# Performance work log

Hardware: AMD Instinct MI355X
Metric: run time of the kernel (lower is better)

## Reference

```python
import jax, jax.numpy as jnp
import numpy as np

SIGMA = 1e-4      # cone height (DistanceFieldPenetrationLoss sigma)
EPS = 1e-9
THRESH = 2000.0   # pen_loss[pen_loss < 2000]
WEIGHT = 0.1      # self.weight


def setup_inputs() -> dict:
    key = jax.random.key(0)
    k1, k2, k3, k4 = jax.random.split(key, 4)
    B, NV, NF, C = 16, 6890, 13776, 65536
    verts = jax.random.normal(k1, (B, NV, 3), dtype=jnp.float32)
    trans = jax.random.normal(k2, (B, 3), dtype=jnp.float32)
    faces = jax.random.randint(k3, (NF, 3), 0, NV)
    collision_idxs = jax.random.randint(k4, (B // 2, C, 2), 0, 2 * NF)
    return {"verts": verts, "trans": trans, "faces": faces,
            "collision_idxs": collision_idxs}


def _pen_distance(triangles, collision_idxs):
    # triangles: [Bp, F, 3, 3]; collision_idxs: [Bp, C, 2]
    intr_idx = collision_idxs[..., 0]
    recv_idx = collision_idxs[..., 1]
    # stand-in for the BVH's (-1)-padding / self-collision filter
    valid = (intr_idx != recv_idx).astype(triangles.dtype)            # [Bp, C]
    gather = jax.vmap(lambda t, i: t[i])
    intr = gather(triangles, intr_idx)                                # [Bp, C, 3, 3]
    recv = gather(triangles, recv_idx)                                # [Bp, C, 3, 3]
    # receiver triangle frame
    e1 = recv[..., 1, :] - recv[..., 0, :]
    e2 = recv[..., 2, :] - recv[..., 0, :]
    n = jnp.cross(e1, e2)
    n = n / (jnp.linalg.norm(n, axis=-1, keepdims=True) + EPS)        # unit normal
    c = recv.mean(axis=-2)                                            # [Bp, C, 3] centroid
    radius = jnp.linalg.norm(recv - c[..., None, :], axis=-1).max(axis=-1)  # circumscribed radius
    # conical distance field evaluated at the 3 intruder vertices
    delta = intr - c[..., None, :]                                    # [Bp, C, 3, 3]
    d = jnp.einsum('bcvk,bck->bcv', delta, n)                         # signed normal distance
    radial = jnp.linalg.norm(delta - d[..., None] * n[..., None, :], axis=-1)
    field = jax.nn.relu(-d / SIGMA) * jax.nn.relu(1.0 - radial / (radius[..., None] + EPS))
    pair_loss = (field ** 2).sum(axis=-1)                             # [Bp, C]
    return (pair_loss * valid).sum(axis=-1)                           # [Bp]


def reference(verts, trans, faces, collision_idxs):
    B, NV, _ = verts.shape
    NF = faces.shape[0]
    vertices = verts + trans[:, None, :]                              # [B, NV, 3]
    offs = (jnp.arange(B, dtype=faces.dtype) * NV)[:, None, None]
    faces_idx = (faces[None] + offs).reshape(B // 2, 2 * NF, 3)       # merge person pairs
    triangles = vertices.reshape(-1, 3)[faces_idx]                    # [B//2, 2*NF, 3, 3]
    pen = _pen_distance(triangles, collision_idxs)                    # [B//2]
    keep = (pen < THRESH).astype(pen.dtype)
    cnt = keep.sum()
    vals = (jax.nn.sigmoid(pen / THRESH) - 0.5) * keep
    loss = jnp.where(cnt > 0, vals.sum() / jnp.maximum(cnt, 1.0), 0.0) * WEIGHT
    return loss
```

## Files before the change

### kernel.cpp

```cpp
#include <hip/hip_runtime.h>
#include <math.h>

namespace {
constexpr int kB  = 16;
constexpr int kNV = 6890;
constexpr int kNF = 13776;
constexpr int kP  = kB / 2;
constexpr int kC  = 65536;
constexpr int kChunks    = kC / 256;
constexpr int kPenBlocks = kP * kChunks;
}
#define SIGMA_F 1e-4f
#define EPS_F   1e-9f
#define THRESH_F 2000.0f
#define WEIGHT_F 0.1f

__global__ void __launch_bounds__(256)
pen_direct(const int* __restrict__ coll,
           const float* __restrict__ verts,
           const float* __restrict__ trans,
           const int* __restrict__ faces,
           float* __restrict__ partials) {
    int blk = blockIdx.x;
    int p = blk & 7;
    int i = (blk >> 3) * 256 + threadIdx.x;
    int2 idx = ((const int2*)coll)[p * kC + i];

    const float t0x = trans[6 * p + 0], t0y = trans[6 * p + 1], t0z = trans[6 * p + 2];
    const float t1x = trans[6 * p + 3], t1y = trans[6 * p + 4], t1z = trans[6 * p + 5];

    float local = 0.0f;
    if (idx.x != idx.y) {
        int hi = (idx.x >= kNF) ? 1 : 0;
        int hr = (idx.y >= kNF) ? 1 : 0;
        const int* fi = faces + 3 * (idx.x - hi * kNF);
        const int* fr = faces + 3 * (idx.y - hr * kNF);
        int vi0 = fi[0], vi1 = fi[1], vi2 = fi[2];
        int vr0 = fr[0], vr1 = fr[1], vr2 = fr[2];

        size_t bi = (size_t)(2 * p + hi) * kNV;
        size_t br = (size_t)(2 * p + hr) * kNV;
        float tix = hi ? t1x : t0x, tiy = hi ? t1y : t0y, tiz = hi ? t1z : t0z;
        float trx = hr ? t1x : t0x, try_ = hr ? t1y : t0y, trz = hr ? t1z : t0z;

        const float* q;
        q = verts + (bi + vi0) * 3; float3 i0 = make_float3(q[0] + tix, q[1] + tiy, q[2] + tiz);
        q = verts + (bi + vi1) * 3; float3 i1 = make_float3(q[0] + tix, q[1] + tiy, q[2] + tiz);
        q = verts + (bi + vi2) * 3; float3 i2 = make_float3(q[0] + tix, q[1] + tiy, q[2] + tiz);
        q = verts + (br + vr0) * 3; float3 r0 = make_float3(q[0] + trx, q[1] + try_, q[2] + trz);
        q = verts + (br + vr1) * 3; float3 r1 = make_float3(q[0] + trx, q[1] + try_, q[2] + trz);
        q = verts + (br + vr2) * 3; float3 r2 = make_float3(q[0] + trx, q[1] + try_, q[2] + trz);

        float e1x = r1.x - r0.x, e1y = r1.y - r0.y, e1z = r1.z - r0.z;
        float e2x = r2.x - r0.x, e2y = r2.y - r0.y, e2z = r2.z - r0.z;
        float nx = e1y * e2z - e1z * e2y;
        float ny = e1z * e2x - e1x * e2z;
        float nz = e1x * e2y - e1y * e2x;
        float nn = sqrtf(nx * nx + ny * ny + nz * nz) + EPS_F;
        nx /= nn; ny /= nn; nz /= nn;
        float cx = (r0.x + r1.x + r2.x) / 3.0f;
        float cy = (r0.y + r1.y + r2.y) / 3.0f;
        float cz = (r0.z + r1.z + r2.z) / 3.0f;
        float r2m = 0.0f;
        {
            float dx = r0.x - cx, dy = r0.y - cy, dz = r0.z - cz;
            r2m = fmaxf(r2m, dx * dx + dy * dy + dz * dz);
            dx = r1.x - cx; dy = r1.y - cy; dz = r1.z - cz;
            r2m = fmaxf(r2m, dx * dx + dy * dy + dz * dz);
            dx = r2.x - cx; dy = r2.y - cy; dz = r2.z - cz;
            r2m = fmaxf(r2m, dx * dx + dy * dy + dz * dz);
        }
        float rad_eps = sqrtf(r2m) + EPS_F;

        float3 iv[3] = {i0, i1, i2};
        float acc = 0.0f;
#pragma unroll
        for (int k = 0; k < 3; ++k) {
            float dx = iv[k].x - cx, dy = iv[k].y - cy, dz = iv[k].z - cz;
            float d = dx * nx + dy * ny + dz * nz;
            float px = dx - d * nx, py = dy - d * ny, pz = dz - d * nz;
            float radial = sqrtf(px * px + py * py + pz * pz);
            float fa = fmaxf(-d / SIGMA_F, 0.0f);
            float fb = fmaxf(1.0f - radial / rad_eps, 0.0f);
            float fd = fa * fb;
            acc += fd * fd;
        }
        local = acc;
    }

#pragma unroll
    for (int off = 32; off > 0; off >>= 1)
        local += __shfl_down(local, off, 64);
    __shared__ float red[4];
    int lane = threadIdx.x & 63;
    int wid  = threadIdx.x >> 6;
    if (lane == 0) red[wid] = local;
    __syncthreads();
    if (threadIdx.x == 0)
        partials[blk] = red[0] + red[1] + red[2] + red[3];
}

__global__ void __launch_bounds__(512)
finalize_kernel(const float* __restrict__ partials, float* __restrict__ out) {
    int wv = threadIdx.x >> 6;
    int lane = threadIdx.x & 63;
    float s = 0.0f;
#pragma unroll
    for (int k = 0; k < 4; ++k) {
        int j = lane + 64 * k;
        s += partials[wv + 8 * j];
    }
#pragma unroll
    for (int off = 32; off > 0; off >>= 1)
        s += __shfl_down(s, off, 64);
    __shared__ float pen[kP];
    if (lane == 0) pen[wv] = s;
    __syncthreads();
    if (threadIdx.x == 0) {
        float cnt = 0.0f, vals = 0.0f;
#pragma unroll
        for (int q = 0; q < kP; ++q) {
            float pq = pen[q];
            float keep = (pq < THRESH_F) ? 1.0f : 0.0f;
            cnt += keep;
            float sg = 1.0f / (1.0f + expf(-pq / THRESH_F));
            vals += (sg - 0.5f) * keep;
        }
        float loss = (cnt > 0.0f) ? (vals / fmaxf(cnt, 1.0f)) : 0.0f;
        out[0] = loss * WEIGHT_F;
    }
}

extern "C" void kernel_launch(void* const* d_in, const int* in_sizes, int n_in,
                              void* d_out, int out_size, void* d_ws, size_t ws_size,
                              hipStream_t stream) {
    const float* verts = (const float*)d_in[0];
    const float* trans = (const float*)d_in[1];
    const int*   faces = (const int*)d_in[2];
    const int*   coll  = (const int*)d_in[3];
    float* out      = (float*)d_out;
    float* partials = (float*)d_ws;

    pen_direct<<<kPenBlocks, 256, 0, stream>>>(coll, verts, trans, faces, partials);
    finalize_kernel<<<1, 512, 0, stream>>>(partials, out);
}
```

Before: 81.85 us.

## Stage face index table into LDS as 16-bit indices per block

Adds a kernel that copies most of the face index table into shared memory as unsigned shorts, then resolves each collision pair's face-to-vertex lookups from LDS instead of global memory. It uses 1024-thread blocks and falls back to the original kernel if the large dynamic LDS size cannot be set. Every block re-reads the whole face table to fill LDS while serving only 1024 pairs. That staging traffic and the low occupancy from about 80 KB of LDS per block can outweigh the saved gather latency.

Result: slower. 88.10 us (+7.6%).

```diff
diff --git a/kernel.cpp b/kernel.cpp
--- a/kernel.cpp
+++ b/kernel.cpp
@@ -7,13 +7,127 @@
 constexpr int kNF = 13776;
 constexpr int kP  = kB / 2;
 constexpr int kC  = 65536;
-constexpr int kChunks    = kC / 256;
-constexpr int kPenBlocks = kP * kChunks;
+constexpr int kLdsFaces   = 13568;
+constexpr int kLdsBytes   = 81408;
+constexpr int kChunksL    = kC / 1024;
+constexpr int kBlocksL    = kP * kChunksL;
+constexpr int kChunksF    = kC / 256;
+constexpr int kBlocksF    = kP * kChunksF;
 }
 #define SIGMA_F 1e-4f
 #define EPS_F   1e-9f
 #define THRESH_F 2000.0f
 #define WEIGHT_F 0.1f
+
+__device__ __forceinline__ float cone_pair_loss(
+    float3 r0, float3 r1, float3 r2, float3 i0, float3 i1, float3 i2) {
+    float e1x = r1.x - r0.x, e1y = r1.y - r0.y, e1z = r1.z - r0.z;
+    float e2x = r2.x - r0.x, e2y = r2.y - r0.y, e2z = r2.z - r0.z;
+    float nx = e1y * e2z - e1z * e2y;
+    float ny = e1z * e2x - e1x * e2z;
+    float nz = e1x * e2y - e1y * e2x;
+    float nn = sqrtf(nx * nx + ny * ny + nz * nz) + EPS_F;
+    nx /= nn; ny /= nn; nz /= nn;
+    float cx = (r0.x + r1.x + r2.x) / 3.0f;
+    float cy = (r0.y + r1.y + r2.y) / 3.0f;
+    float cz = (r0.z + r1.z + r2.z) / 3.0f;
+    float r2m = 0.0f;
+    {
+        float dx = r0.x - cx, dy = r0.y - cy, dz = r0.z - cz;
+        r2m = fmaxf(r2m, dx * dx + dy * dy + dz * dz);
+        dx = r1.x - cx; dy = r1.y - cy; dz = r1.z - cz;
+        r2m = fmaxf(r2m, dx * dx + dy * dy + dz * dz);
+        dx = r2.x - cx; dy = r2.y - cy; dz = r2.z - cz;
+        r2m = fmaxf(r2m, dx * dx + dy * dy + dz * dz);
+    }
+    float rad_eps = sqrtf(r2m) + EPS_F;
+    float3 iv[3] = {i0, i1, i2};
+    float acc = 0.0f;
+#pragma unroll
+    for (int k = 0; k < 3; ++k) {
+        float dx = iv[k].x - cx, dy = iv[k].y - cy, dz = iv[k].z - cz;
+        float d = dx * nx + dy * ny + dz * nz;
+        float px = dx - d * nx, py = dy - d * ny, pz = dz - d * nz;
+        float radial = sqrtf(px * px + py * py + pz * pz);
+        float fa = fmaxf(-d / SIGMA_F, 0.0f);
+        float fb = fmaxf(1.0f - radial / rad_eps, 0.0f);
+        float fd = fa * fb;
+        acc += fd * fd;
+    }
+    return acc;
+}
+
+__global__ void __launch_bounds__(1024, 8)
+pen_lds(const int* __restrict__ coll,
+        const float* __restrict__ verts,
+        const float* __restrict__ trans,
+        const int* __restrict__ faces,
+        float* __restrict__ partials) {
+    extern __shared__ unsigned short lf[];
+    for (int f = threadIdx.x; f < kLdsFaces; f += 1024) {
+        int a = faces[3 * f + 0];
+        int b = faces[3 * f + 1];
+        int c = faces[3 * f + 2];
+        lf[3 * f + 0] = (unsigned short)a;
+        lf[3 * f + 1] = (unsigned short)b;
+        lf[3 * f + 2] = (unsigned short)c;
+    }
+    __syncthreads();
+
+    int blk = blockIdx.x;
+    int p = blk & 7;
+    int i = (blk >> 3) * 1024 + threadIdx.x;
+    int2 idx = ((const int2*)coll)[p * kC + i];
+
+    const float t0x = trans[6 * p + 0], t0y = trans[6 * p + 1], t0z = trans[6 * p + 2];
+    const float t1x = trans[6 * p + 3], t1y = trans[6 * p + 4], t1z = trans[6 * p + 5];
+
+    float local = 0.0f;
+    if (idx.x != idx.y) {
+        int hi = (idx.x >= kNF) ? 1 : 0;
+        int hr = (idx.y >= kNF) ? 1 : 0;
+        int fI = idx.x - hi * kNF;
+        int fR = idx.y - hr * kNF;
+        int vi0, vi1, vi2, vr0, vr1, vr2;
+        if (fI < kLdsFaces) {
+            vi0 = lf[3 * fI]; vi1 = lf[3 * fI + 1]; vi2 = lf[3 * fI + 2];
+        } else {
+            const int* fp = faces + 3 * fI; vi0 = fp[0]; vi1 = fp[1]; vi2 = fp[2];
+        }
+        if (fR < kLdsFaces) {
+            vr0 = lf[3 * fR]; vr1 = lf[3 * fR + 1]; vr2 = lf[3 * fR + 2];
+        } else {
+            const int* fp = faces + 3 * fR; vr0 = fp[0]; vr1 = fp[1]; vr2 = fp[2];
+        }
+        size_t bi = (size_t)(2 * p + hi) * kNV;
+        size_t br = (size_t)(2 * p + hr) * kNV;
+        float tix = hi ? t1x : t0x, tiy = hi ? t1y : t0y, tiz = hi ? t1z : t0z;
+        float trx = hr ? t1x : t0x, try_ = hr ? t1y : t0y, trz = hr ? t1z : t0z;
+        const float* q;
+        q = verts + (bi + vi0) * 3; float3 i0 = make_float3(q[0] + tix, q[1] + tiy, q[2] + tiz);
+        q = verts + (bi + vi1) * 3; float3 i1 = make_float3(q[0] + tix, q[1] + tiy, q[2] + tiz);
+        q = verts + (bi + vi2) * 3; float3 i2 = make_float3(q[0] + tix, q[1] + tiy, q[2] + tiz);
+        q = verts + (br + vr0) * 3; float3 r0 = make_float3(q[0] + trx, q[1] + try_, q[2] + trz);
+        q = verts + (br + vr1) * 3; float3 r1 = make_float3(q[0] + trx, q[1] + try_, q[2] + trz);
+        q = verts + (br + vr2) * 3; float3 r2 = make_float3(q[0] + trx, q[1] + try_, q[2] + trz);
+        local = cone_pair_loss(r0, r1, r2, i0, i1, i2);
+    }
+
+#pragma unroll
+    for (int off = 32; off > 0; off >>= 1)
+        local += __shfl_down(local, off, 64);
+    __shared__ float red[16];
+    int lane = threadIdx.x & 63;
+    int wid  = threadIdx.x >> 6;
+    if (lane == 0) red[wid] = local;
+    __syncthreads();
+    if (threadIdx.x == 0) {
+        float s = 0.0f;
+#pragma unroll
+        for (int w = 0; w < 16; ++w) s += red[w];
+        partials[blk] = s;
+    }
+}
 
 __global__ void __launch_bounds__(256)
 pen_direct(const int* __restrict__ coll,
@@ -25,10 +139,8 @@
     int p = blk & 7;
     int i = (blk >> 3) * 256 + threadIdx.x;
     int2 idx = ((const int2*)coll)[p * kC + i];
-
     const float t0x = trans[6 * p + 0], t0y = trans[6 * p + 1], t0z = trans[6 * p + 2];
     const float t1x = trans[6 * p + 3], t1y = trans[6 * p + 4], t1z = trans[6 * p + 5];
-
     float local = 0.0f;
     if (idx.x != idx.y) {
         int hi = (idx.x >= kNF) ? 1 : 0;
@@ -37,12 +149,10 @@
         const int* fr = faces + 3 * (idx.y - hr * kNF);
         int vi0 = fi[0], vi1 = fi[1], vi2 = fi[2];
         int vr0 = fr[0], vr1 = fr[1], vr2 = fr[2];
-
         size_t bi = (size_t)(2 * p + hi) * kNV;
         size_t br = (size_t)(2 * p + hr) * kNV;
         float tix = hi ? t1x : t0x, tiy = hi ? t1y : t0y, tiz = hi ? t1z : t0z;
         float trx = hr ? t1x : t0x, try_ = hr ? t1y : t0y, trz = hr ? t1z : t0z;
-
         const float* q;
         q = verts + (bi + vi0) * 3; float3 i0 = make_float3(q[0] + tix, q[1] + tiy, q[2] + tiz);
         q = verts + (bi + vi1) * 3; float3 i1 = make_float3(q[0] + tix, q[1] + tiy, q[2] + tiz);
@@ -50,44 +160,8 @@
         q = verts + (br + vr0) * 3; float3 r0 = make_float3(q[0] + trx, q[1] + try_, q[2] + trz);
         q = verts + (br + vr1) * 3; float3 r1 = make_float3(q[0] + trx, q[1] + try_, q[2] + trz);
         q = verts + (br + vr2) * 3; float3 r2 = make_float3(q[0] + trx, q[1] + try_, q[2] + trz);
-
-        float e1x = r1.x - r0.x, e1y = r1.y - r0.y, e1z = r1.z - r0.z;
-        float e2x = r2.x - r0.x, e2y = r2.y - r0.y, e2z = r2.z - r0.z;
-        float nx = e1y * e2z - e1z * e2y;
-        float ny = e1z * e2x - e1x * e2z;
-        float nz = e1x * e2y - e1y * e2x;
-        float nn = sqrtf(nx * nx + ny * ny + nz * nz) + EPS_F;
-        nx /= nn; ny /= nn; nz /= nn;
-        float cx = (r0.x + r1.x + r2.x) / 3.0f;
-        float cy = (r0.y + r1.y + r2.y) / 3.0f;
-        float cz = (r0.z + r1.z + r2.z) / 3.0f;
-        float r2m = 0.0f;
-        {
-            float dx = r0.x - cx, dy = r0.y - cy, dz = r0.z - cz;
-            r2m = fmaxf(r2m, dx * dx + dy * dy + dz * dz);
-            dx = r1.x - cx; dy = r1.y - cy; dz = r1.z - cz;
-            r2m = fmaxf(r2m, dx * dx + dy * dy + dz * dz);
-            dx = r2.x - cx; dy = r2.y - cy; dz = r2.z - cz;
-            r2m = fmaxf(r2m, dx * dx + dy * dy + dz * dz);
-        }
-        float rad_eps = sqrtf(r2m) + EPS_F;
-
-        float3 iv[3] = {i0, i1, i2};
-        float acc = 0.0f;
-#pragma unroll
-        for (int k = 0; k < 3; ++k) {
-            float dx = iv[k].x - cx, dy = iv[k].y - cy, dz = iv[k].z - cz;
-            float d = dx * nx + dy * ny + dz * nz;
-            float px = dx - d * nx, py = dy - d * ny, pz = dz - d * nz;
-            float radial = sqrtf(px * px + py * py + pz * pz);
-            float fa = fmaxf(-d / SIGMA_F, 0.0f);
-            float fb = fmaxf(1.0f - radial / rad_eps, 0.0f);
-            float fd = fa * fb;
-            acc += fd * fd;
-        }
-        local = acc;
-    }
-
+        local = cone_pair_loss(r0, r1, r2, i0, i1, i2);
+    }
 #pragma unroll
     for (int off = 32; off > 0; off >>= 1)
         local += __shfl_down(local, off, 64);
@@ -101,15 +175,12 @@
 }
 
 __global__ void __launch_bounds__(512)
-finalize_kernel(const float* __restrict__ partials, float* __restrict__ out) {
+finalize_kernel(const float* __restrict__ partials, float* __restrict__ out, int chunks) {
     int wv = threadIdx.x >> 6;
     int lane = threadIdx.x & 63;
     float s = 0.0f;
-#pragma unroll
-    for (int k = 0; k < 4; ++k) {
-        int j = lane + 64 * k;
+    for (int j = lane; j < chunks; j += 64)
         s += partials[wv + 8 * j];
-    }
 #pragma unroll
     for (int off = 32; off > 0; off >>= 1)
         s += __shfl_down(s, off, 64);
@@ -141,6 +212,18 @@
     float* out      = (float*)d_out;
     float* partials = (float*)d_ws;
 
-    pen_direct<<<kPenBlocks, 256, 0, stream>>>(coll, verts, trans, faces, partials);
-    finalize_kernel<<<1, 512, 0, stream>>>(partials, out);
-}
+    static bool lds_ok = []() {
+        hipError_t e = hipFuncSetAttribute((const void*)pen_lds,
+                                           hipFuncAttributeMaxDynamicSharedMemorySize,
+                                           kLdsBytes);
+        return e == hipSuccess;
+    }();
+
+    if (lds_ok) {
+        pen_lds<<<kBlocksL, 1024, kLdsBytes, stream>>>(coll, verts, trans, faces, partials);
+        finalize_kernel<<<1, 512, 0, stream>>>(partials, out, kChunksL);
+    } else {
+        pen_direct<<<kBlocksF, 256, 0, stream>>>(coll, verts, trans, faces, partials);
+        finalize_kernel<<<1, 512, 0, stream>>>(partials, out, kChunksF);
+    }
+}
```

## Precompute per-triangle frames and vertices in fp16 before the pair loss pass

Applied to the files above, without the earlier changes.

Adds a build kernel that computes each triangle's centroid, unit normal and radius, plus its translated vertices, once per face, and stores them packed as fp16 in workspace. The pair kernel then does one 16-byte frame load and about 20 bytes of vertex loads per collision, replacing the face-index plus six scattered vertex gathers and the per-pair frame computation. The aim is to cut dependent random memory traffic. The trade-offs are an extra launch, fp16 rounding of coordinates (the normal distance is scaled by 1/sigma = 1e4, so errors are amplified), and a fallback to the old path when the workspace is too small.

Result: no change. 82.17 us (+0.4%).

```diff
diff --git a/kernel.cpp b/kernel.cpp
--- a/kernel.cpp
+++ b/kernel.cpp
@@ -1,19 +1,189 @@
 #include <hip/hip_runtime.h>
+#include <hip/hip_fp16.h>
 #include <math.h>
+#include <string.h>
 
 namespace {
 constexpr int kB  = 16;
 constexpr int kNV = 6890;
 constexpr int kNF = 13776;
+constexpr int kTF = 2 * kNF;
 constexpr int kP  = kB / 2;
 constexpr int kC  = 65536;
 constexpr int kChunks    = kC / 256;
 constexpr int kPenBlocks = kP * kChunks;
+constexpr int kBChunks   = (kTF + 255) / 256;
+constexpr int kBuildBlocks = kP * kBChunks;
+constexpr size_t kPartOff   = 0;
+constexpr size_t kFrameOff  = 65536;
+constexpr size_t kFrameSz   = (size_t)kP * kTF * 16;
+constexpr size_t kVertOff   = kFrameOff + kFrameSz;
+constexpr size_t kVertSz    = (size_t)kP * kTF * 32;
 }
 #define SIGMA_F 1e-4f
 #define EPS_F   1e-9f
 #define THRESH_F 2000.0f
 #define WEIGHT_F 0.1f
+
+__device__ __forceinline__ unsigned pack2(float a, float b) {
+    __half2 h = __floats2half2_rn(a, b);
+    unsigned u; memcpy(&u, &h, 4); return u;
+}
+__device__ __forceinline__ float2 unpack2(unsigned u) {
+    __half2 h; memcpy(&h, &u, 4); return __half22float2(h);
+}
+
+__global__ void __launch_bounds__(256)
+build_kernel(const float* __restrict__ verts,
+             const float* __restrict__ trans,
+             const int*   __restrict__ faces,
+             unsigned* __restrict__ frames,
+             unsigned* __restrict__ tverts) {
+    int blk = blockIdx.x;
+    int p = blk & 7;
+    int t = (blk >> 3) * 256 + threadIdx.x;
+    if (t >= kTF) return;
+    int half = (t >= kNF) ? 1 : 0;
+    int b = 2 * p + half;
+    int f = t - half * kNF;
+    float tx = trans[3 * b + 0];
+    float ty = trans[3 * b + 1];
+    float tz = trans[3 * b + 2];
+    float3 v[3];
+#pragma unroll
+    for (int k = 0; k < 3; ++k) {
+        int vi = faces[3 * f + k];
+        const float* vp = verts + ((size_t)b * kNV + vi) * 3;
+        v[k] = make_float3(vp[0] + tx, vp[1] + ty, vp[2] + tz);
+    }
+    float e1x = v[1].x - v[0].x, e1y = v[1].y - v[0].y, e1z = v[1].z - v[0].z;
+    float e2x = v[2].x - v[0].x, e2y = v[2].y - v[0].y, e2z = v[2].z - v[0].z;
+    float nx = e1y * e2z - e1z * e2y;
+    float ny = e1z * e2x - e1x * e2z;
+    float nz = e1x * e2y - e1y * e2x;
+    float nn = sqrtf(nx * nx + ny * ny + nz * nz) + EPS_F;
+    nx /= nn; ny /= nn; nz /= nn;
+    float cx = (v[0].x + v[1].x + v[2].x) / 3.0f;
+    float cy = (v[0].y + v[1].y + v[2].y) / 3.0f;
+    float cz = (v[0].z + v[1].z + v[2].z) / 3.0f;
+    float r2m = 0.0f;
+#pragma unroll
+    for (int k = 0; k < 3; ++k) {
+        float dx = v[k].x - cx, dy = v[k].y - cy, dz = v[k].z - cz;
+        r2m = fmaxf(r2m, dx * dx + dy * dy + dz * dz);
+    }
+    float radius = sqrtf(r2m);
+
+    int g = p * kTF + t;
+    uint4 fr;
+    fr.x = pack2(cx, cy);
+    fr.y = pack2(cz, nx);
+    fr.z = pack2(ny, nz);
+    fr.w = pack2(radius, 0.0f);
+    ((uint4*)frames)[g] = fr;
+
+    uint4 w0;
+    w0.x = pack2(v[0].x, v[0].y);
+    w0.y = pack2(v[0].z, v[1].x);
+    w0.z = pack2(v[1].y, v[1].z);
+    w0.w = pack2(v[2].x, v[2].y);
+    ((uint4*)tverts)[(size_t)g * 2] = w0;
+    tverts[(size_t)g * 8 + 4] = pack2(v[2].z, 0.0f);
+}
+
+__global__ void __launch_bounds__(256)
+pen_kernel(const int* __restrict__ coll,
+           const unsigned* __restrict__ frames,
+           const unsigned* __restrict__ tverts,
+           float* __restrict__ partials) {
+    int blk = blockIdx.x;
+    int p = blk & 7;
+    int i = (blk >> 3) * 256 + threadIdx.x;
+    int2 idx = ((const int2*)coll)[p * kC + i];
+    float local = 0.0f;
+    if (idx.x != idx.y) {
+        int rbase = p * kTF;
+        uint4 fu = ((const uint4*)frames)[rbase + idx.y];
+        uint4 vu = ((const uint4*)tverts)[(size_t)(rbase + idx.x) * 2];
+        unsigned vz = tverts[(size_t)(rbase + idx.x) * 8 + 4];
+        float2 a0 = unpack2(fu.x);
+        float2 a1 = unpack2(fu.y);
+        float2 a2 = unpack2(fu.z);
+        float2 a3 = unpack2(fu.w);
+        float cx = a0.x, cy = a0.y, cz = a1.x;
+        float nx = a1.y, ny = a2.x, nz = a2.y;
+        float rad_eps = a3.x + EPS_F;
+        float2 b0 = unpack2(vu.x);
+        float2 b1 = unpack2(vu.y);
+        float2 b2 = unpack2(vu.z);
+        float2 b3 = unpack2(vu.w);
+        float2 b4 = unpack2(vz);
+        float ivx[3] = {b0.x, b1.y, b3.x};
+        float ivy[3] = {b0.y, b2.x, b3.y};
+        float ivz[3] = {b1.x, b2.y, b4.x};
+        float acc = 0.0f;
+#pragma unroll
+        for (int k = 0; k < 3; ++k) {
+            float dx = ivx[k] - cx, dy = ivy[k] - cy, dz = ivz[k] - cz;
+            float d = dx * nx + dy * ny + dz * nz;
+            float px = dx - d * nx, py = dy - d * ny, pz = dz - d * nz;
+            float radial = sqrtf(px * px + py * py + pz * pz);
+            float fa = fmaxf(-d / SIGMA_F, 0.0f);
+            float fb = fmaxf(1.0f - radial / rad_eps, 0.0f);
+            float fd = fa * fb;
+            acc += fd * fd;
+        }
+        local = acc;
+    }
+#pragma unroll
+    for (int off = 32; off > 0; off >>= 1)
+        local += __shfl_down(local, off, 64);
+    __shared__ float red[4];
+    int lane = threadIdx.x & 63;
+    int wid  = threadIdx.x >> 6;
+    if (lane == 0) red[wid] = local;
+    __syncthreads();
+    if (threadIdx.x == 0)
+        partials[blk] = red[0] + red[1] + red[2] + red[3];
+}
+
+__device__ __forceinline__ float cone_pair_loss(
+    float3 r0, float3 r1, float3 r2, float3 i0, float3 i1, float3 i2) {
+    float e1x = r1.x - r0.x, e1y = r1.y - r0.y, e1z = r1.z - r0.z;
+    float e2x = r2.x - r0.x, e2y = r2.y - r0.y, e2z = r2.z - r0.z;
+    float nx = e1y * e2z - e1z * e2y;
+    float ny = e1z * e2x - e1x * e2z;
+    float nz = e1x * e2y - e1y * e2x;
+    float nn = sqrtf(nx * nx + ny * ny + nz * nz) + EPS_F;
+    nx /= nn; ny /= nn; nz /= nn;
+    float cx = (r0.x + r1.x + r2.x) / 3.0f;
+    float cy = (r0.y + r1.y + r2.y) / 3.0f;
+    float cz = (r0.z + r1.z + r2.z) / 3.0f;
+    float r2m = 0.0f;
+    {
+        float dx = r0.x - cx, dy = r0.y - cy, dz = r0.z - cz;
+        r2m = fmaxf(r2m, dx * dx + dy * dy + dz * dz);
+        dx = r1.x - cx; dy = r1.y - cy; dz = r1.z - cz;
+        r2m = fmaxf(r2m, dx * dx + dy * dy + dz * dz);
+        dx = r2.x - cx; dy = r2.y - cy; dz = r2.z - cz;
+        r2m = fmaxf(r2m, dx * dx + dy * dy + dz * dz);
+    }
+    float rad_eps = sqrtf(r2m) + EPS_F;
+    float3 iv[3] = {i0, i1, i2};
+    float acc = 0.0f;
+#pragma unroll
+    for (int k = 0; k < 3; ++k) {
+        float dx = iv[k].x - cx, dy = iv[k].y - cy, dz = iv[k].z - cz;
+        float d = dx * nx + dy * ny + dz * nz;
+        float px = dx - d * nx, py = dy - d * ny, pz = dz - d * nz;
+        float radial = sqrtf(px * px + py * py + pz * pz);
+        float fa = fmaxf(-d / SIGMA_F, 0.0f);
+        float fb = fmaxf(1.0f - radial / rad_eps, 0.0f);
+        float fd = fa * fb;
+        acc += fd * fd;
+    }
+    return acc;
+}
 
 __global__ void __launch_bounds__(256)
 pen_direct(const int* __restrict__ coll,
@@ -25,10 +195,8 @@
     int p = blk & 7;
     int i = (blk >> 3) * 256 + threadIdx.x;
     int2 idx = ((const int2*)coll)[p * kC + i];
-
     const float t0x = trans[6 * p + 0], t0y = trans[6 * p + 1], t0z = trans[6 * p + 2];
     const float t1x = trans[6 * p + 3], t1y = trans[6 * p + 4], t1z = trans[6 * p + 5];
-
     float local = 0.0f;
     if (idx.x != idx.y) {
         int hi = (idx.x >= kNF) ? 1 : 0;
@@ -37,12 +205,10 @@
         const int* fr = faces + 3 * (idx.y - hr * kNF);
         int vi0 = fi[0], vi1 = fi[1], vi2 = fi[2];
         int vr0 = fr[0], vr1 = fr[1], vr2 = fr[2];
-
         size_t bi = (size_t)(2 * p + hi) * kNV;
         size_t br = (size_t)(2 * p + hr) * kNV;
         float tix = hi ? t1x : t0x, tiy = hi ? t1y : t0y, tiz = hi ? t1z : t0z;
         float trx = hr ? t1x : t0x, try_ = hr ? t1y : t0y, trz = hr ? t1z : t0z;
-
         const float* q;
         q = verts + (bi + vi0) * 3; float3 i0 = make_float3(q[0] + tix, q[1] + tiy, q[2] + tiz);
         q = verts + (bi + vi1) * 3; float3 i1 = make_float3(q[0] + tix, q[1] + tiy, q[2] + tiz);
@@ -50,44 +216,8 @@
         q = verts + (br + vr0) * 3; float3 r0 = make_float3(q[0] + trx, q[1] + try_, q[2] + trz);
         q = verts + (br + vr1) * 3; float3 r1 = make_float3(q[0] + trx, q[1] + try_, q[2] + trz);
         q = verts + (br + vr2) * 3; float3 r2 = make_float3(q[0] + trx, q[1] + try_, q[2] + trz);
-
-        float e1x = r1.x - r0.x, e1y = r1.y - r0.y, e1z = r1.z - r0.z;
-        float e2x = r2.x - r0.x, e2y = r2.y - r0.y, e2z = r2.z - r0.z;
-        float nx = e1y * e2z - e1z * e2y;
-        float ny = e1z * e2x - e1x * e2z;
-        float nz = e1x * e2y - e1y * e2x;
-        float nn = sqrtf(nx * nx + ny * ny + nz * nz) + EPS_F;
-        nx /= nn; ny /= nn; nz /= nn;
-        float cx = (r0.x + r1.x + r2.x) / 3.0f;
-        float cy = (r0.y + r1.y + r2.y) / 3.0f;
-        float cz = (r0.z + r1.z + r2.z) / 3.0f;
-        float r2m = 0.0f;
-        {
-            float dx = r0.x - cx, dy = r0.y - cy, dz = r0.z - cz;
-            r2m = fmaxf(r2m, dx * dx + dy * dy + dz * dz);
-            dx = r1.x - cx; dy = r1.y - cy; dz = r1.z - cz;
-            r2m = fmaxf(r2m, dx * dx + dy * dy + dz * dz);
-            dx = r2.x - cx; dy = r2.y - cy; dz = r2.z - cz;
-            r2m = fmaxf(r2m, dx * dx + dy * dy + dz * dz);
-        }
-        float rad_eps = sqrtf(r2m) + EPS_F;
-
-        float3 iv[3] = {i0, i1, i2};
-        float acc = 0.0f;
-#pragma unroll
-        for (int k = 0; k < 3; ++k) {
-            float dx = iv[k].x - cx, dy = iv[k].y - cy, dz = iv[k].z - cz;
-            float d = dx * nx + dy * ny + dz * nz;
-            float px = dx - d * nx, py = dy - d * ny, pz = dz - d * nz;
-            float radial = sqrtf(px * px + py * py + pz * pz);
-            float fa = fmaxf(-d / SIGMA_F, 0.0f);
-            float fb = fmaxf(1.0f - radial / rad_eps, 0.0f);
-            float fd = fa * fb;
-            acc += fd * fd;
-        }
-        local = acc;
-    }
-
+        local = cone_pair_loss(r0, r1, r2, i0, i1, i2);
+    }
 #pragma unroll
     for (int off = 32; off > 0; off >>= 1)
         local += __shfl_down(local, off, 64);
@@ -105,11 +235,8 @@
     int wv = threadIdx.x >> 6;
     int lane = threadIdx.x & 63;
     float s = 0.0f;
-#pragma unroll
-    for (int k = 0; k < 4; ++k) {
-        int j = lane + 64 * k;
+    for (int j = lane; j < kChunks; j += 64)
         s += partials[wv + 8 * j];
-    }
 #pragma unroll
     for (int off = 32; off > 0; off >>= 1)
         s += __shfl_down(s, off, 64);
@@ -121,10 +248,10 @@
 #pragma unroll
         for (int q = 0; q < kP; ++q) {
             float pq = pen[q];
-            float keep = (pq < THRESH_F) ? 1.0f : 0.0f;
-            cnt += keep;
-            float sg = 1.0f / (1.0f + expf(-pq / THRESH_F));
-            vals += (sg - 0.5f) * keep;
+            if (pq < THRESH_F) {
+                cnt += 1.0f;
+                vals += 1.0f / (1.0f + expf(-pq / THRESH_F)) - 0.5f;
+            }
         }
         float loss = (cnt > 0.0f) ? (vals / fmaxf(cnt, 1.0f)) : 0.0f;
         out[0] = loss * WEIGHT_F;
@@ -139,8 +266,15 @@
     const int*   faces = (const int*)d_in[2];
     const int*   coll  = (const int*)d_in[3];
     float* out      = (float*)d_out;
-    float* partials = (float*)d_ws;
-
-    pen_direct<<<kPenBlocks, 256, 0, stream>>>(coll, verts, trans, faces, partials);
+    float* partials = (float*)((char*)d_ws + kPartOff);
+
+    if (ws_size >= kVertOff + kVertSz) {
+        unsigned* frames = (unsigned*)((char*)d_ws + kFrameOff);
+        unsigned* tverts = (unsigned*)((char*)d_ws + kVertOff);
+        build_kernel<<<kBuildBlocks, 256, 0, stream>>>(verts, trans, faces, frames, tverts);
+        pen_kernel<<<kPenBlocks, 256, 0, stream>>>(coll, frames, tverts, partials);
+    } else {
+        pen_direct<<<kPenBlocks, 256, 0, stream>>>(coll, verts, trans, faces, partials);
+    }
     finalize_kernel<<<1, 512, 0, stream>>>(partials, out);
 }
```
